# Kernel tuning notes

Measured on AMD Instinct MI355X. Metric: run time of the kernel, lower is better.

Reference implementation:

```python
import jax, jax.numpy as jnp
import numpy as np

TOP_K = 2
NUM_EXPERTS = 8
LB_COEFF = 0.01


def setup_inputs() -> dict:
    key = jax.random.key(0)
    ks = jax.random.split(key, 5)
    B, S, D, F, E = 4, 2048, 1024, 4096, NUM_EXPERTS
    s_in = 0.02
    return {
        "x": jax.random.normal(ks[0], (B, S, D), jnp.float32),
        "gate_w": jax.random.normal(ks[1], (D, E), jnp.float32) * s_in,
        "gate_b": jnp.zeros((E,), jnp.float32),
        "fc1_w": jax.random.normal(ks[2], (E, D, 2 * F), jnp.float32) * s_in,
        "fc1_b": jnp.zeros((E, 2 * F), jnp.float32),
        "fc2_w": jax.random.normal(ks[3], (E, F, D), jnp.float32) * s_in,
        "fc2_b": jnp.zeros((E, D), jnp.float32),
    }


def reference(x, gate_w, gate_b, fc1_w, fc1_b, fc2_w, fc2_b):
    B, S, D = x.shape
    E = gate_w.shape[1]
    xt = x.reshape(-1, D)                      # [T, D]
    T = xt.shape[0]

    gate_logits = xt @ gate_w + gate_b        # [T, E]
    gate_probs = jax.nn.softmax(gate_logits, axis=-1)
    top_w, top_i = jax.lax.top_k(gate_probs, TOP_K)      # [T, K]
    w_norm = top_w / (top_w.sum(-1, keepdims=True) + 1e-6)

    rows = jnp.arange(T)[:, None]
    # per-token per-expert combine weight (0 if expert not in top-k)
    combine = jnp.zeros((T, E), xt.dtype).at[rows, top_i].add(w_norm)  # [T, E]

    out = jnp.zeros_like(xt)
    for e in range(E):  # fixed small expert loop; each is a dense GEMM
        h = xt @ fc1_w[e] + fc1_b[e]                      # [T, 2F]
        a, g = jnp.split(h, 2, axis=-1)
        act = a * jax.nn.gelu(g, approximate=False)       # SwiGLU (exact gelu, torch default)
        y = act @ fc2_w[e] + fc2_b[e]                     # [T, D]
        out = out + combine[:, e:e + 1] * y

    chosen_mask = jnp.zeros((T, E), gate_probs.dtype).at[rows, top_i].set(1.0)
    frac = chosen_mask.mean(0)
    mean_probs = gate_probs.mean(0)
    lb_loss = LB_COEFF * E * jnp.sum(frac * mean_probs)

    return out.reshape(B, S, D), lb_loss
```

## Files before the change

kernel.cpp:

```cpp
#include <hip/hip_runtime.h>
#include <hip/hip_bf16.h>
#include <stdint.h>

typedef __attribute__((ext_vector_type(4))) float f32x4;
typedef __attribute__((ext_vector_type(16))) float f32x16;
typedef __attribute__((ext_vector_type(8))) __bf16 bf16x8;
typedef __attribute__((ext_vector_type(4))) unsigned short u16x4;
typedef unsigned short u16;

#define NTOK 8192
#define DDIM 1024
#define FDIM 4096
#define NEXP 8
#define NT1 144

#define WS_XB    0ull
#define WS_W1T   (16777216ull)
#define WS_W2T   (WS_W1T + 134217728ull)
#define WS_ACT   (WS_W2T + 67108864ull)
#define WS_LIST  (WS_ACT + 142606336ull)
#define WS_PAIRW (WS_LIST + 262144ull)
#define WS_CNT   (WS_PAIRW + 262144ull)
#define WS_SUMP  (WS_CNT + 32ull)
#define WS_PAD   (WS_SUMP + 32ull)
#define WS_OFF   (WS_PAD + 32ull)
#define WS_T1E   (WS_OFF + 32ull)
#define WS_T1R   (WS_T1E + 1024ull)
#define WS_SE    (WS_T1R + 1024ull)
#define WS_SP    (WS_SE + 65536ull)

static __device__ __forceinline__ u16 bf16rne(float f) {
  union { float f; uint32_t u; } c; c.f = f;
  return (u16)((c.u + 0x7FFFu + ((c.u >> 16) & 1u)) >> 16);
}

static __device__ __forceinline__ void load_lds16(const void* g, void* l) {
  __builtin_amdgcn_global_load_lds((const __attribute__((address_space(1))) void*)g,
                                   (__attribute__((address_space(3))) void*)l, 16, 0, 0);
}

__global__ __launch_bounds__(256) void gate_kernel(
    const float* __restrict__ x, const float* __restrict__ gw,
    const float* __restrict__ gb, u16* __restrict__ xb,
    int* __restrict__ cnt, float* __restrict__ sump,
    int* __restrict__ list, float* __restrict__ pairw,
    int* __restrict__ slotE, int* __restrict__ slotP) {
  const int tid = threadIdx.x;
  const int lane = tid & 63;
  const int wv = tid >> 6;
  const int t = blockIdx.x * 4 + wv;

  __shared__ float sp[8];
  if (tid < 8) sp[tid] = 0.f;
  __syncthreads();

  float acc[8] = {0.f,0.f,0.f,0.f,0.f,0.f,0.f,0.f};
  const float4* x4 = (const float4*)x + (size_t)t * 256;
  u16x4* xb4 = (u16x4*)xb + (size_t)t * 256;
  #pragma unroll
  for (int it = 0; it < 4; ++it) {
    const float4 xv = x4[it * 64 + lane];
    u16x4 bv;
    bv[0] = bf16rne(xv.x); bv[1] = bf16rne(xv.y);
    bv[2] = bf16rne(xv.z); bv[3] = bf16rne(xv.w);
    xb4[it * 64 + lane] = bv;
    const int d0 = (it * 64 + lane) * 4;
    #pragma unroll
    for (int j = 0; j < 4; ++j) {
      const float xs = (j == 0) ? xv.x : ((j == 1) ? xv.y : ((j == 2) ? xv.z : xv.w));
      const float* g = gw + (size_t)(d0 + j) * 8;
      #pragma unroll
      for (int e2 = 0; e2 < 8; ++e2) acc[e2] += xs * g[e2];
    }
  }
  #pragma unroll
  for (int e2 = 0; e2 < 8; ++e2) {
    float v = acc[e2];
    v += __shfl_xor(v, 1);  v += __shfl_xor(v, 2);  v += __shfl_xor(v, 4);
    v += __shfl_xor(v, 8);  v += __shfl_xor(v, 16); v += __shfl_xor(v, 32);
    acc[e2] = v;
  }
  float p[8]; float mx = -1e30f;
  #pragma unroll
  for (int e2 = 0; e2 < 8; ++e2) { p[e2] = acc[e2] + gb[e2]; mx = fmaxf(mx, p[e2]); }
  float s = 0.f;
  #pragma unroll
  for (int e2 = 0; e2 < 8; ++e2) { p[e2] = expf(p[e2] - mx); s += p[e2]; }
  const float inv = 1.f / s;
  #pragma unroll
  for (int e2 = 0; e2 < 8; ++e2) p[e2] *= inv;

  if (lane == 0) {
    int i1 = 0; float v1 = p[0];
    #pragma unroll
    for (int e2 = 1; e2 < 8; ++e2) if (p[e2] > v1) { v1 = p[e2]; i1 = e2; }
    int i2 = 0; float v2 = -1.f;
    #pragma unroll
    for (int e2 = 0; e2 < 8; ++e2) if (e2 != i1 && p[e2] > v2) { v2 = p[e2]; i2 = e2; }
    const float den = v1 + v2 + 1e-6f;
    const int p1 = atomicAdd(&cnt[i1], 1);
    list[i1 * NTOK + p1] = t; pairw[i1 * NTOK + p1] = v1 / den;
    slotE[2 * t] = i1; slotP[2 * t] = p1;
    const int p2 = atomicAdd(&cnt[i2], 1);
    list[i2 * NTOK + p2] = t; pairw[i2 * NTOK + p2] = v2 / den;
    slotE[2 * t + 1] = i2; slotP[2 * t + 1] = p2;
    #pragma unroll
    for (int e2 = 0; e2 < 8; ++e2) atomicAdd(&sp[e2], p[e2]);
  }
  __syncthreads();
  if (tid < 8) atomicAdd(&sump[tid], sp[tid]);
}

__global__ __launch_bounds__(256) void conv_transpose(
    const float* __restrict__ in, u16* __restrict__ out, int R, int C) {
  __shared__ float tile[64][65];
  const int e = blockIdx.z;
  const float* pin = in + (size_t)e * R * C;
  u16* pout = out + (size_t)e * R * C;
  const int tx = threadIdx.x & 15;
  const int ty = threadIdx.x >> 4;
  const int c0 = blockIdx.x * 64;
  const int r0 = blockIdx.y * 64;
  #pragma unroll
  for (int i = 0; i < 4; ++i) {
    const int r = ty + i * 16;
    const float4 v = *(const float4*)(pin + (size_t)(r0 + r) * C + c0 + tx * 4);
    tile[r][tx * 4 + 0] = v.x;
    tile[r][tx * 4 + 1] = v.y;
    tile[r][tx * 4 + 2] = v.z;
    tile[r][tx * 4 + 3] = v.w;
  }
  __syncthreads();
  #pragma unroll
  for (int i = 0; i < 4; ++i) {
    const int c = ty + i * 16;
    u16x4 o;
    o[0] = bf16rne(tile[tx * 4 + 0][c]);
    o[1] = bf16rne(tile[tx * 4 + 1][c]);
    o[2] = bf16rne(tile[tx * 4 + 2][c]);
    o[3] = bf16rne(tile[tx * 4 + 3][c]);
    *(u16x4*)(pout + (size_t)(c0 + c) * R + r0 + tx * 4) = o;
  }
}

__global__ void route_finalize(const int* __restrict__ cnt, const float* __restrict__ sump,
                               int* __restrict__ padc, int* __restrict__ offs,
                               int* __restrict__ list, float* __restrict__ pairw,
                               int* __restrict__ t1e, int* __restrict__ t1r,
                               float* __restrict__ lb_out) {
  __shared__ int s_c[8], s_p[8];
  const int tid = threadIdx.x;
  if (tid == 0) {
    int o = 0; float lb = 0.f;
    for (int e = 0; e < 8; ++e) {
      const int c = cnt[e];
      const int pc = (c + 127) & ~127;
      s_c[e] = c; s_p[e] = pc;
      padc[e] = pc; offs[e] = o; o += pc;
      lb += ((float)c / 8192.f) * (sump[e] / 8192.f);
    }
    lb_out[0] = 0.01f * 8.f * lb;
    int n1 = 0;
    for (int e = 0; e < 8; ++e)
      for (int r = 0; r < s_p[e]; r += 128) { t1e[n1] = e; t1r[n1] = r; ++n1; }
    for (; n1 < NT1; ++n1) { t1e[n1] = -1; t1r[n1] = 0; }
  }
  __syncthreads();
  for (int e = 0; e < 8; ++e)
    for (int pq = s_c[e] + tid; pq < s_p[e]; pq += blockDim.x) {
      list[e * NTOK + pq] = 0; pairw[e * NTOK + pq] = 0.f;
    }
}

__global__ __launch_bounds__(256) void gemm1_kernel(
    const u16* __restrict__ xb, const u16* __restrict__ w1t,
    const float* __restrict__ b1, const int* __restrict__ list,
    const int* __restrict__ offs,
    const int* __restrict__ t1e, const int* __restrict__ t1r,
    u16* __restrict__ act) {
  const int tt = blockIdx.y;
  const int e = t1e[tt];
  if (e < 0) return;
  const int row0 = t1r[tt];
  const int j = blockIdx.x;
  const int off_e = offs[e];

  __shared__ u16 lds[24576];

  const int tid = threadIdx.x;
  const int lane = tid & 63;
  const int wv = tid >> 6;
  const int wr = wv >> 1, wc = wv & 1;
  const int l31 = lane & 31, s5 = lane >> 5;

  const int rt = tid >> 2;
  const int ce = ((tid & 3) ^ ((rt >> 1) & 3)) * 8;
  const int tok0 = list[e * NTOK + row0 + rt];
  const int tok1 = list[e * NTOK + row0 + rt + 64];
  const u16* srcA0 = xb + (size_t)tok0 * DDIM + ce;
  const u16* srcA1 = xb + (size_t)tok1 * DDIM + ce;
  const u16* srcB[4];
  #pragma unroll
  for (int seg = 0; seg < 4; ++seg) {
    const int rb = rt + seg * 64;
    const int q = rb >> 5;
    const int gn = j * 128 + (q >> 1) * 32 + (rb & 31) + (q & 1) * FDIM;
    srcB[seg] = w1t + ((size_t)e * 2 * FDIM + gn) * DDIM + ce;
  }

  const int xsw = (l31 >> 1) & 3;
  const int kel0 = (s5 ^ xsw) * 8;
  const int aB0 = (wr * 64 + l31) * 32 + kel0;   const int aB1 = aB0 ^ 16;
  const int bB0 = (wc * 128 + l31) * 32 + kel0;  const int bB1 = bB0 ^ 16;

  f32x16 acc[2][4];
  #pragma unroll
  for (int m = 0; m < 2; ++m)
    #pragma unroll
    for (int n = 0; n < 4; ++n)
      #pragma unroll
      for (int i = 0; i < 16; ++i) acc[m][n][i] = 0.f;

  #define STAGE1(buf, kt) do { \
    u16* _dA = &lds[(buf) * 4096 + wv * 512]; \
    u16* _dB = &lds[8192 + (buf) * 8192 + wv * 512]; \
    load_lds16(srcA0 + (kt) * 32, _dA); \
    load_lds16(srcA1 + (kt) * 32, _dA + 2048); \
    load_lds16(srcB[0] + (kt) * 32, _dB); \
    load_lds16(srcB[1] + (kt) * 32, _dB + 2048); \
    load_lds16(srcB[2] + (kt) * 32, _dB + 4096); \
    load_lds16(srcB[3] + (kt) * 32, _dB + 6144); \
  } while (0)

  STAGE1(0, 0);
  for (int kt = 0; kt < DDIM / 32; ++kt) {
    const int cur = kt & 1;
    __syncthreads();
    if (kt + 1 < DDIM / 32) STAGE1(cur ^ 1, kt + 1);
    const int bA = cur * 4096;
    const int bB = 8192 + cur * 8192;
    bf16x8 a0[2], a1[2], Bh0[4], Bh1[4];
    #pragma unroll
    for (int m = 0; m < 2; ++m) {
      a0[m] = *(const bf16x8*)&lds[bA + aB0 + m * 1024];
      a1[m] = *(const bf16x8*)&lds[bA + aB1 + m * 1024];
    }
    #pragma unroll
    for (int n = 0; n < 4; ++n) {
      Bh0[n] = *(const bf16x8*)&lds[bB + bB0 + n * 1024];
      Bh1[n] = *(const bf16x8*)&lds[bB + bB1 + n * 1024];
    }
    #pragma unroll
    for (int m = 0; m < 2; ++m)
      #pragma unroll
      for (int n = 0; n < 4; ++n) {
        acc[m][n] = __builtin_amdgcn_mfma_f32_32x32x16_bf16(a0[m], Bh0[n], acc[m][n], 0, 0, 0);
        acc[m][n] = __builtin_amdgcn_mfma_f32_32x32x16_bf16(a1[m], Bh1[n], acc[m][n], 0, 0, 0);
      }
  }
  #undef STAGE1

  const size_t actrow0 = (size_t)(off_e + row0);
  #pragma unroll
  for (int p2 = 0; p2 < 2; ++p2) {
    const int col = j * 128 + wc * 64 + p2 * 32 + l31;
    const float ba = b1[e * (2 * FDIM) + col];
    const float bg = b1[e * (2 * FDIM) + FDIM + col];
    #pragma unroll
    for (int m = 0; m < 2; ++m) {
      #pragma unroll
      for (int r = 0; r < 16; ++r) {
        const int row = wr * 64 + m * 32 + (r & 3) + 8 * (r >> 2) + 4 * s5;
        const float a = acc[m][2 * p2][r] + ba;
        const float g = acc[m][2 * p2 + 1][r] + bg;
        const float u2 = 1.5957691216057308f * (g + 0.044715f * g * g * g);
        const float sg = 1.f / (1.f + __expf(-u2));
        act[(actrow0 + row) * FDIM + col] = bf16rne(a * g * sg);
      }
    }
  }
}

__global__ __launch_bounds__(256) void gemm2_kernel(
    const u16* __restrict__ act, const u16* __restrict__ w2t,
    const float* __restrict__ b2, const float* __restrict__ pairw,
    const int* __restrict__ offs,
    const int* __restrict__ t1e, const int* __restrict__ t1r,
    float* __restrict__ y) {
  const int bid = blockIdx.x;
  const int r8 = bid & 7;
  const int q = bid >> 3;
  const int jt = q & 7;
  const int tt = (q >> 3) * 8 + r8;
  const int e = t1e[tt];
  if (e < 0) return;
  const int row0 = t1r[tt];
  const int off_e = offs[e];

  __shared__ u16 lds[16384];

  const int tid = threadIdx.x;
  const int lane = tid & 63;
  const int wv = tid >> 6;
  const int wr = wv >> 1, wc = wv & 1;
  const int l31 = lane & 31, s5 = lane >> 5;

  const int rt = tid >> 2;
  const int ce = ((tid & 3) ^ ((rt >> 1) & 3)) * 8;
  const u16* srcA0 = act + (size_t)(off_e + row0 + rt) * FDIM + ce;
  const u16* srcA1 = act + (size_t)(off_e + row0 + rt + 64) * FDIM + ce;
  const u16* srcB0 = w2t + ((size_t)e * DDIM + jt * 128 + rt) * FDIM + ce;
  const u16* srcB1 = w2t + ((size_t)e * DDIM + jt * 128 + rt + 64) * FDIM + ce;

  const int xsw = (l31 >> 1) & 3;
  const int kel0 = (s5 ^ xsw) * 8;
  const int aB0 = (wr * 64 + l31) * 32 + kel0;  const int aB1 = aB0 ^ 16;
  const int bB0 = (wc * 64 + l31) * 32 + kel0;  const int bB1 = bB0 ^ 16;

  f32x16 acc[2][2];
  #pragma unroll
  for (int m = 0; m < 2; ++m)
    #pragma unroll
    for (int n = 0; n < 2; ++n)
      #pragma unroll
      for (int i = 0; i < 16; ++i) acc[m][n][i] = 0.f;

  #define STAGE2(buf, kt) do { \
    u16* _dA = &lds[(buf) * 4096 + wv * 512]; \
    u16* _dB = &lds[8192 + (buf) * 4096 + wv * 512]; \
    load_lds16(srcA0 + (kt) * 32, _dA); \
    load_lds16(srcA1 + (kt) * 32, _dA + 2048); \
    load_lds16(srcB0 + (kt) * 32, _dB); \
    load_lds16(srcB1 + (kt) * 32, _dB + 2048); \
  } while (0)

  STAGE2(0, 0);
  for (int kt = 0; kt < FDIM / 32; ++kt) {
    const int cur = kt & 1;
    __syncthreads();
    if (kt + 1 < FDIM / 32) STAGE2(cur ^ 1, kt + 1);
    const int bA = cur * 4096;
    const int bB = 8192 + cur * 4096;
    bf16x8 a0[2], a1[2], Bh0[2], Bh1[2];
    #pragma unroll
    for (int m = 0; m < 2; ++m) {
      a0[m] = *(const bf16x8*)&lds[bA + aB0 + m * 1024];
      a1[m] = *(const bf16x8*)&lds[bA + aB1 + m * 1024];
    }
    #pragma unroll
    for (int n = 0; n < 2; ++n) {
      Bh0[n] = *(const bf16x8*)&lds[bB + bB0 + n * 1024];
      Bh1[n] = *(const bf16x8*)&lds[bB + bB1 + n * 1024];
    }
    #pragma unroll
    for (int m = 0; m < 2; ++m)
      #pragma unroll
      for (int n = 0; n < 2; ++n) {
        acc[m][n] = __builtin_amdgcn_mfma_f32_32x32x16_bf16(a0[m], Bh0[n], acc[m][n], 0, 0, 0);
        acc[m][n] = __builtin_amdgcn_mfma_f32_32x32x16_bf16(a1[m], Bh1[n], acc[m][n], 0, 0, 0);
      }
  }
  #undef STAGE2

  #pragma unroll
  for (int m = 0; m < 2; ++m) {
    #pragma unroll
    for (int r = 0; r < 16; ++r) {
      const int row = wr * 64 + m * 32 + (r & 3) + 8 * (r >> 2) + 4 * s5;
      const int pos = row0 + row;
      const float pw = pairw[e * NTOK + pos];
      if (pw != 0.f) {
        float* yr = y + (size_t)(off_e + pos) * DDIM;
        #pragma unroll
        for (int n = 0; n < 2; ++n) {
          const int col = jt * 128 + wc * 64 + n * 32 + l31;
          yr[col] = (acc[m][n][r] + b2[e * DDIM + col]) * pw;
        }
      }
    }
  }
}

__global__ __launch_bounds__(256) void gather_kernel(
    const float* __restrict__ y, const int* __restrict__ slotE,
    const int* __restrict__ slotP, const int* __restrict__ offs,
    float* __restrict__ out) {
  const int t = blockIdx.x * 4 + (threadIdx.x >> 6);
  const int lane = threadIdx.x & 63;
  const int r1 = offs[slotE[2 * t]] + slotP[2 * t];
  const int r2 = offs[slotE[2 * t + 1]] + slotP[2 * t + 1];
  const float4* y1 = (const float4*)(y + (size_t)r1 * DDIM);
  const float4* y2 = (const float4*)(y + (size_t)r2 * DDIM);
  float4* o4 = (float4*)(out + (size_t)t * DDIM);
  #pragma unroll
  for (int i = 0; i < 4; ++i) {
    const float4 a = y1[i * 64 + lane];
    const float4 b = y2[i * 64 + lane];
    float4 r; r.x = a.x + b.x; r.y = a.y + b.y; r.z = a.z + b.z; r.w = a.w + b.w;
    o4[i * 64 + lane] = r;
  }
}

extern "C" void kernel_launch(void* const* d_in, const int* in_sizes, int n_in,
                              void* d_out, int out_size, void* d_ws, size_t ws_size,
                              hipStream_t stream) {
  const float* x   = (const float*)d_in[0];
  const float* gw  = (const float*)d_in[1];
  const float* gb  = (const float*)d_in[2];
  const float* f1w = (const float*)d_in[3];
  const float* f1b = (const float*)d_in[4];
  const float* f2w = (const float*)d_in[5];
  const float* f2b = (const float*)d_in[6];
  float* out = (float*)d_out;
  char* ws = (char*)d_ws;

  u16*   xb    = (u16*)(ws + WS_XB);
  u16*   w1t   = (u16*)(ws + WS_W1T);
  float* y     = (float*)(ws + WS_W1T);
  u16*   w2t   = (u16*)(ws + WS_W2T);
  u16*   act   = (u16*)(ws + WS_ACT);
  int*   list  = (int*)(ws + WS_LIST);
  float* pairw = (float*)(ws + WS_PAIRW);
  int*   cnt   = (int*)(ws + WS_CNT);
  float* sump  = (float*)(ws + WS_SUMP);
  int*   padc  = (int*)(ws + WS_PAD);
  int*   offs  = (int*)(ws + WS_OFF);
  int*   t1e   = (int*)(ws + WS_T1E);
  int*   t1r   = (int*)(ws + WS_T1R);
  int*   slotE = (int*)(ws + WS_SE);
  int*   slotP = (int*)(ws + WS_SP);

  (void)hipMemsetAsync(ws + WS_CNT, 0, 64, stream);

  gate_kernel<<<NTOK / 4, 256, 0, stream>>>(x, gw, gb, xb, cnt, sump, list, pairw, slotE, slotP);
  conv_transpose<<<dim3(8192 / 64, 1024 / 64, 8), 256, 0, stream>>>(f1w, w1t, 1024, 8192);
  conv_transpose<<<dim3(1024 / 64, 4096 / 64, 8), 256, 0, stream>>>(f2w, w2t, 4096, 1024);
  route_finalize<<<1, 256, 0, stream>>>(cnt, sump, padc, offs, list, pairw,
                                        t1e, t1r, out + 8388608);
  gemm1_kernel<<<dim3(32, NT1), 256, 0, stream>>>(xb, w1t, f1b, list, offs, t1e, t1r, act);
  gemm2_kernel<<<NT1 * 8, 256, 0, stream>>>(act, w2t, f2b, pairw, offs, t1e, t1r, y);
  gather_kernel<<<NTOK / 4, 256, 0, stream>>>(y, slotE, slotP, offs, out);
}
```

Before: 932.8 us.

## Split-K gemm2 into two halves with bf16 partial outputs summed in gather

The second expert GEMM's K dimension is split into two halves, which doubles the number of blocks so more CUs are busy. Each half writes a bf16 partial result to its own buffer, with the bias added only in the first half. The gather kernel then sums four bf16 partials per token instead of two fp32 rows. This trades extra partial-output traffic and bf16 rounding of the outputs for more parallelism in gemm2 and about the same byte volume as before.

```diff
diff --git a/kernel.cpp b/kernel.cpp
--- a/kernel.cpp
+++ b/kernel.cpp
@@ -6,6 +6,7 @@
 typedef __attribute__((ext_vector_type(16))) float f32x16;
 typedef __attribute__((ext_vector_type(8))) __bf16 bf16x8;
 typedef __attribute__((ext_vector_type(4))) unsigned short u16x4;
+typedef __attribute__((ext_vector_type(8))) unsigned short u16x8;
 typedef unsigned short u16;
 
 #define NTOK 8192
@@ -13,6 +14,7 @@
 #define FDIM 4096
 #define NEXP 8
 #define NT1 144
+#define YHALF 17825792ull
 
 #define WS_XB    0ull
 #define WS_W1T   (16777216ull)
@@ -32,6 +34,11 @@
 static __device__ __forceinline__ u16 bf16rne(float f) {
   union { float f; uint32_t u; } c; c.f = f;
   return (u16)((c.u + 0x7FFFu + ((c.u >> 16) & 1u)) >> 16);
+}
+
+static __device__ __forceinline__ float bf16tof(u16 v) {
+  union { uint32_t u; float f; } c; c.u = ((uint32_t)v) << 16;
+  return c.f;
 }
 
 static __device__ __forceinline__ void load_lds16(const void* g, void* l) {
@@ -286,12 +293,13 @@
     const float* __restrict__ b2, const float* __restrict__ pairw,
     const int* __restrict__ offs,
     const int* __restrict__ t1e, const int* __restrict__ t1r,
-    float* __restrict__ y) {
+    u16* __restrict__ y) {
   const int bid = blockIdx.x;
   const int r8 = bid & 7;
   const int q = bid >> 3;
   const int jt = q & 7;
-  const int tt = (q >> 3) * 8 + r8;
+  const int ks = (q >> 3) & 1;
+  const int tt = (q >> 4) * 8 + r8;
   const int e = t1e[tt];
   if (e < 0) return;
   const int row0 = t1r[tt];
@@ -307,10 +315,11 @@
 
   const int rt = tid >> 2;
   const int ce = ((tid & 3) ^ ((rt >> 1) & 3)) * 8;
-  const u16* srcA0 = act + (size_t)(off_e + row0 + rt) * FDIM + ce;
-  const u16* srcA1 = act + (size_t)(off_e + row0 + rt + 64) * FDIM + ce;
-  const u16* srcB0 = w2t + ((size_t)e * DDIM + jt * 128 + rt) * FDIM + ce;
-  const u16* srcB1 = w2t + ((size_t)e * DDIM + jt * 128 + rt + 64) * FDIM + ce;
+  const int k0 = ks * 2048;
+  const u16* srcA0 = act + (size_t)(off_e + row0 + rt) * FDIM + k0 + ce;
+  const u16* srcA1 = act + (size_t)(off_e + row0 + rt + 64) * FDIM + k0 + ce;
+  const u16* srcB0 = w2t + ((size_t)e * DDIM + jt * 128 + rt) * FDIM + k0 + ce;
+  const u16* srcB1 = w2t + ((size_t)e * DDIM + jt * 128 + rt + 64) * FDIM + k0 + ce;
 
   const int xsw = (l31 >> 1) & 3;
   const int kel0 = (s5 ^ xsw) * 8;
@@ -335,10 +344,10 @@
   } while (0)
 
   STAGE2(0, 0);
-  for (int kt = 0; kt < FDIM / 32; ++kt) {
+  for (int kt = 0; kt < 64; ++kt) {
     const int cur = kt & 1;
     __syncthreads();
-    if (kt + 1 < FDIM / 32) STAGE2(cur ^ 1, kt + 1);
+    if (kt + 1 < 64) STAGE2(cur ^ 1, kt + 1);
     const int bA = cur * 4096;
     const int bB = 8192 + cur * 4096;
     bf16x8 a0[2], a1[2], Bh0[2], Bh1[2];
@@ -362,6 +371,7 @@
   }
   #undef STAGE2
 
+  u16* yk = y + (size_t)ks * YHALF;
   #pragma unroll
   for (int m = 0; m < 2; ++m) {
     #pragma unroll
@@ -370,11 +380,12 @@
       const int pos = row0 + row;
       const float pw = pairw[e * NTOK + pos];
       if (pw != 0.f) {
-        float* yr = y + (size_t)(off_e + pos) * DDIM;
+        u16* yr = yk + (size_t)(off_e + pos) * DDIM;
         #pragma unroll
         for (int n = 0; n < 2; ++n) {
           const int col = jt * 128 + wc * 64 + n * 32 + l31;
-          yr[col] = (acc[m][n][r] + b2[e * DDIM + col]) * pw;
+          const float bb = ks ? 0.f : b2[e * DDIM + col];
+          yr[col] = bf16rne((acc[m][n][r] + bb) * pw);
         }
       }
     }
@@ -382,22 +393,35 @@
 }
 
 __global__ __launch_bounds__(256) void gather_kernel(
-    const float* __restrict__ y, const int* __restrict__ slotE,
+    const u16* __restrict__ y, const int* __restrict__ slotE,
     const int* __restrict__ slotP, const int* __restrict__ offs,
     float* __restrict__ out) {
   const int t = blockIdx.x * 4 + (threadIdx.x >> 6);
   const int lane = threadIdx.x & 63;
   const int r1 = offs[slotE[2 * t]] + slotP[2 * t];
   const int r2 = offs[slotE[2 * t + 1]] + slotP[2 * t + 1];
-  const float4* y1 = (const float4*)(y + (size_t)r1 * DDIM);
-  const float4* y2 = (const float4*)(y + (size_t)r2 * DDIM);
+  const u16x8* ya = (const u16x8*)(y + (size_t)r1 * DDIM);
+  const u16x8* yb = (const u16x8*)(y + YHALF + (size_t)r1 * DDIM);
+  const u16x8* yc = (const u16x8*)(y + (size_t)r2 * DDIM);
+  const u16x8* yd = (const u16x8*)(y + YHALF + (size_t)r2 * DDIM);
   float4* o4 = (float4*)(out + (size_t)t * DDIM);
   #pragma unroll
-  for (int i = 0; i < 4; ++i) {
-    const float4 a = y1[i * 64 + lane];
-    const float4 b = y2[i * 64 + lane];
-    float4 r; r.x = a.x + b.x; r.y = a.y + b.y; r.z = a.z + b.z; r.w = a.w + b.w;
-    o4[i * 64 + lane] = r;
+  for (int i = 0; i < 2; ++i) {
+    const u16x8 a = ya[i * 64 + lane];
+    const u16x8 b = yb[i * 64 + lane];
+    const u16x8 c = yc[i * 64 + lane];
+    const u16x8 d = yd[i * 64 + lane];
+    float4 r0, r1f;
+    r0.x = bf16tof(a[0]) + bf16tof(b[0]) + bf16tof(c[0]) + bf16tof(d[0]);
+    r0.y = bf16tof(a[1]) + bf16tof(b[1]) + bf16tof(c[1]) + bf16tof(d[1]);
+    r0.z = bf16tof(a[2]) + bf16tof(b[2]) + bf16tof(c[2]) + bf16tof(d[2]);
+    r0.w = bf16tof(a[3]) + bf16tof(b[3]) + bf16tof(c[3]) + bf16tof(d[3]);
+    r1f.x = bf16tof(a[4]) + bf16tof(b[4]) + bf16tof(c[4]) + bf16tof(d[4]);
+    r1f.y = bf16tof(a[5]) + bf16tof(b[5]) + bf16tof(c[5]) + bf16tof(d[5]);
+    r1f.z = bf16tof(a[6]) + bf16tof(b[6]) + bf16tof(c[6]) + bf16tof(d[6]);
+    r1f.w = bf16tof(a[7]) + bf16tof(b[7]) + bf16tof(c[7]) + bf16tof(d[7]);
+    o4[(i * 64 + lane) * 2]     = r0;
+    o4[(i * 64 + lane) * 2 + 1] = r1f;
   }
 }
 
@@ -416,7 +440,7 @@
 
   u16*   xb    = (u16*)(ws + WS_XB);
   u16*   w1t   = (u16*)(ws + WS_W1T);
-  float* y     = (float*)(ws + WS_W1T);
+  u16*   y     = (u16*)(ws + WS_W1T);
   u16*   w2t   = (u16*)(ws + WS_W2T);
   u16*   act   = (u16*)(ws + WS_ACT);
   int*   list  = (int*)(ws + WS_LIST);
@@ -438,6 +462,6 @@
   route_finalize<<<1, 256, 0, stream>>>(cnt, sump, padc, offs, list, pairw,
                                         t1e, t1r, out + 8388608);
   gemm1_kernel<<<dim3(32, NT1), 256, 0, stream>>>(xb, w1t, f1b, list, offs, t1e, t1r, act);
-  gemm2_kernel<<<NT1 * 8, 256, 0, stream>>>(act, w2t, f2b, pairw, offs, t1e, t1r, y);
+  gemm2_kernel<<<NT1 * 16, 256, 0, stream>>>(act, w2t, f2b, pairw, offs, t1e, t1r, y);
   gather_kernel<<<NTOK / 4, 256, 0, stream>>>(y, slotE, slotP, offs, out);
 }
```

Result: no change. 942.7 us (+1.1%).
